# Kernel tuning notes

Measured on AMD Instinct MI355X. Metric: run time of the kernel, lower is better.

Reference implementation:

```python
import jax, jax.numpy as jnp
import numpy as np

E = 1024          # n_embed_dim
H = 64            # head_size = n_embed_dim // n_heads (16)

def setup_inputs() -> dict:
    key = jax.random.key(0)
    k_x, k_q, k_k, k_v = jax.random.split(key, 4)
    scale = 1.0 / np.sqrt(E)
    return {
        "x": jax.random.normal(k_x, (4, 2048, E), dtype=jnp.float32),
        "ln_gamma": jnp.ones((E,), jnp.float32),
        "ln_beta": jnp.zeros((E,), jnp.float32),
        # torch nn.Linear weights: [out_features, in_features]
        "Wq": jax.random.normal(k_q, (H, E), dtype=jnp.float32) * scale,
        "Wk": jax.random.normal(k_k, (H, E), dtype=jnp.float32) * scale,
        "Wv": jax.random.normal(k_v, (H, E), dtype=jnp.float32) * scale,
    }

def reference(x, ln_gamma, ln_beta, Wq, Wk, Wv):
    # LayerNorm over last dim (eps matches torch default 1e-5)
    mu = jnp.mean(x, axis=-1, keepdims=True)
    var = jnp.mean(jnp.square(x - mu), axis=-1, keepdims=True)
    xn = (x - mu) * jax.lax.rsqrt(var + 1e-5) * ln_gamma + ln_beta

    q = jnp.einsum('bse,he->bsh', xn, Wq)   # [B,S,H]
    k = jnp.einsum('bse,he->bsh', xn, Wk)
    v = jnp.einsum('bse,he->bsh', xn, Wv)

    scores = jnp.einsum('bqh,bkh->bqk', q, k) / jnp.sqrt(jnp.float32(H))
    S = x.shape[1]
    causal = jnp.tril(jnp.ones((S, S), dtype=bool))
    scores = jnp.where(causal, scores, -jnp.inf)
    attn = jax.nn.softmax(scores, axis=-1)
    return jnp.einsum('bqk,bkh->bqh', attn, v)
```

## Files before the change

kernel.cpp:

```cpp
#include <hip/hip_runtime.h>

#define E 1024
#define HH 64
#define BB 4
#define SS 2048
#define BS (BB*SS)
#define NSLOT 144

typedef unsigned short u16;
typedef short bf16x8 __attribute__((ext_vector_type(8)));
typedef float f32x4 __attribute__((ext_vector_type(4)));

#define LOG2E_O8 0.18033688011112042f

__device__ inline u16 f2bf(float f) {
    unsigned int u = __float_as_uint(f);
    unsigned int r = (u + 0x7FFFu + ((u >> 16) & 1u)) >> 16;
    return (u16)r;
}
__device__ inline float bf2f(u16 h) {
    return __uint_as_float(((unsigned int)h) << 16);
}
__device__ inline void gl2lds(const u16* g, u16* l) {
    __builtin_amdgcn_global_load_lds(
        (const __attribute__((address_space(1))) unsigned int*)g,
        (__attribute__((address_space(3))) unsigned int*)l,
        16, 0, 0);
}

__global__ __launch_bounds__(256) void ln_wcast(const float* __restrict__ x,
        const float* __restrict__ gamma, const float* __restrict__ beta,
        const float* __restrict__ Wq, const float* __restrict__ Wk,
        const float* __restrict__ Wv,
        u16* __restrict__ xn, u16* __restrict__ wc) {
    const int t = threadIdx.x;
    if (blockIdx.x < 2048) {
        const int w = t >> 6, lane = t & 63;
        const size_t row = (size_t)blockIdx.x * 4 + w;
        const int r7 = (int)(row & 7);
        const float4* xr = (const float4*)(x + row * E);
        float4 v[4];
        #pragma unroll
        for (int i = 0; i < 4; ++i) v[i] = xr[lane + 64 * i];
        float s = 0.f, sq = 0.f;
        #pragma unroll
        for (int i = 0; i < 4; ++i) {
            s  += v[i].x + v[i].y + v[i].z + v[i].w;
            sq += v[i].x*v[i].x + v[i].y*v[i].y + v[i].z*v[i].z + v[i].w*v[i].w;
        }
        #pragma unroll
        for (int off = 32; off > 0; off >>= 1) {
            s  += __shfl_xor(s,  off);
            sq += __shfl_xor(sq, off);
        }
        const float mean = s * (1.0f / E);
        const float var  = sq * (1.0f / E) - mean * mean;
        const float rstd = rsqrtf(var + 1e-5f);
        const float4* gr = (const float4*)gamma;
        const float4* br = (const float4*)beta;
        #pragma unroll
        for (int i = 0; i < 4; ++i) {
            const float4 g  = gr[lane + 64 * i];
            const float4 bt = br[lane + 64 * i];
            ushort4 o;
            o.x = f2bf((v[i].x - mean) * rstd * g.x + bt.x);
            o.y = f2bf((v[i].y - mean) * rstd * g.y + bt.y);
            o.z = f2bf((v[i].z - mean) * rstd * g.z + bt.z);
            o.w = f2bf((v[i].w - mean) * rstd * g.w + bt.w);
            const int p = lane + 64 * i;
            const int dst = (p >> 5) * 128 + ((p >> 4) & 1) * 64
                          + ((((p >> 1) & 7) ^ r7) * 8) + (p & 1) * 4;
            *(ushort4*)(xn + row * E + dst) = o;
        }
    } else {
        const int row = blockIdx.x - 2048;
        const float* src = (row < 64)  ? (Wq + (size_t)row * E)
                         : (row < 128) ? (Wk + (size_t)(row - 64) * E)
                                       : (Wv + (size_t)(row - 128) * E);
        const float sc = (row < 64) ? LOG2E_O8 : 1.0f;
        const float4 v = *(const float4*)(src + t * 4);
        ushort4 o;
        o.x = f2bf(v.x * sc); o.y = f2bf(v.y * sc);
        o.z = f2bf(v.z * sc); o.w = f2bf(v.w * sc);
        const int dst = (t >> 5) * 128 + ((t >> 4) & 1) * 64
                      + ((((t >> 1) & 7) ^ (row & 7)) * 8) + (t & 1) * 4;
        *(ushort4*)(wc + (size_t)row * E + dst) = o;
    }
}

__global__ __launch_bounds__(256) void qkv_mfma(const u16* __restrict__ xn,
        const u16* __restrict__ wc,
        u16* __restrict__ qb, u16* __restrict__ kb, u16* __restrict__ vt) {
    const int mb   = blockIdx.x >> 1;
    const int half = blockIdx.x & 1;
    const int row0 = mb * 32;
    const int t = threadIdx.x;
    const int w = t >> 6, lane = t & 63;
    const int quad = lane >> 4, r15 = lane & 15;
    const int mt = w >> 1, cgrp = w & 1;
    __shared__ u16 Xs[2][32 * 128];
    __shared__ u16 Ws[2][96 * 128];
    f32x4 acc[3] = {};
    const int xrow = mt * 16 + r15;

    const int srow = t >> 4, u = t & 15;

    auto stage = [&](int kc, int buf) {
        gl2lds(xn + (size_t)(row0 + srow) * E + kc * 128 + u * 8,
               &Xs[buf][w * 512]);
        gl2lds(xn + (size_t)(row0 + 16 + srow) * E + kc * 128 + u * 8,
               &Xs[buf][2048 + w * 512]);
        #pragma unroll
        for (int i = 0; i < 6; ++i) {
            const int wl = i * 16 + srow;
            gl2lds(wc + (size_t)(half * 96 + wl) * E + kc * 128 + u * 8,
                   &Ws[buf][i * 2048 + w * 512]);
        }
    };

    stage(0, 0);
    __syncthreads();

    for (int kc8 = 0; kc8 < 8; ++kc8) {
        const int cur = kc8 & 1;
        if (kc8 < 7) stage(kc8 + 1, cur ^ 1);
        #pragma unroll
        for (int kk = 0; kk < 4; ++kk) {
            const int hf = kk >> 1, q4 = (kk & 1) * 4 + quad;
            const bf16x8 af = *(const bf16x8*)&Xs[cur][xrow * 128 + hf * 64 + (q4 ^ (xrow & 7)) * 8];
            #pragma unroll
            for (int j = 0; j < 3; ++j) {
                const int wl = (cgrp * 3 + j) * 16 + r15;
                const bf16x8 bfr = *(const bf16x8*)&Ws[cur][wl * 128 + hf * 64 + (q4 ^ (wl & 7)) * 8];
                acc[j] = __builtin_amdgcn_mfma_f32_16x16x32_bf16(af, bfr, acc[j], 0, 0, 0);
            }
        }
        __syncthreads();
    }

    const int b    = row0 >> 11;
    const int key0 = row0 & 2047;
    #pragma unroll
    for (int j = 0; j < 3; ++j) {
        const int cg  = half * 96 + cgrp * 48 + j * 16 + r15;
        const int sel = cg >> 6;
        const int col = cg & 63;
        if (sel < 2) {
            u16* base = (sel == 0) ? qb : kb;
            #pragma unroll
            for (int r = 0; r < 4; ++r) {
                const size_t row = (size_t)row0 + mt * 16 + quad * 4 + r;
                base[row * HH + col] = f2bf(acc[j][r]);
            }
        } else {
            ushort4 pk;
            pk.x = f2bf(acc[j][0]); pk.y = f2bf(acc[j][1]);
            pk.z = f2bf(acc[j][2]); pk.w = f2bf(acc[j][3]);
            *(ushort4*)(vt + (size_t)b * HH * SS + (size_t)col * SS
                           + key0 + mt * 16 + quad * 4) = pk;
        }
    }
}

__global__ __launch_bounds__(256) void attn_partial(const u16* __restrict__ qb,
        const u16* __restrict__ kb, const u16* __restrict__ vt,
        u16* __restrict__ po, float* __restrict__ pl,
        float* __restrict__ out) {
    const int bid = blockIdx.x;
    const int b   = bid / 72;
    const int s2  = bid - b * 72;
    int a = (int)((sqrtf(4.0f * s2 + 1.0f) - 1.0f) * 0.5f);
    while ((a + 1) * (a + 2) <= s2) ++a;
    while (a * (a + 1) > s2) --a;
    const int rem = s2 - a * (a + 1);
    const int rp  = rem / (a + 1);
    const int c   = rem - rp * (a + 1);
    const int qt0 = 4 * a + 2 * rp;
    const int nc  = a + 1;
    const int t = threadIdx.x;
    const int w = t >> 6, lane = t & 63;
    const int quad = lane >> 4, r15 = lane & 15;

    __shared__ u16 Ks[4 * 64 * 64];
    __shared__ u16 VT[4 * 64 * 64];
    __shared__ u16 Ps[64 * 64];

    bf16x8 qf0[2], qf1[2];
    #pragma unroll
    for (int qi = 0; qi < 2; ++qi) {
        const size_t qrow = ((size_t)b * SS + (qt0 + qi) * 64 + w * 16 + r15) * HH;
        qf0[qi] = *(const bf16x8*)(qb + qrow + quad * 8);
        qf1[qi] = *(const bf16x8*)(qb + qrow + 32 + quad * 8);
    }

    const int ntmax = (c < a) ? 4 : (2 * rp + 2);

    {
        const int row = t >> 2, ch0 = (t & 3) * 2;
        for (int tl = 0; tl < ntmax; ++tl) {
            const int kt = (c * 4 + tl) << 6;
            const uint4* srcK = (const uint4*)(kb + ((size_t)b * SS + kt + row) * HH + ch0 * 8);
            const uint4 k0 = srcK[0], k1 = srcK[1];
            *(uint4*)&Ks[tl * 4096 + row * 64 + ((ch0    ) ^ (row & 7)) * 8] = k0;
            *(uint4*)&Ks[tl * 4096 + row * 64 + ((ch0 + 1) ^ (row & 7)) * 8] = k1;
            const uint4* srcV = (const uint4*)(vt + (size_t)b * HH * SS + (size_t)row * SS
                                               + kt + ch0 * 8);
            const uint4 v0 = srcV[0], v1 = srcV[1];
            *(uint4*)&VT[tl * 4096 + row * 64 + ((ch0    ) ^ (row & 7)) * 8] = v0;
            *(uint4*)&VT[tl * 4096 + row * 64 + ((ch0 + 1) ^ (row & 7)) * 8] = v1;
        }
    }
    __syncthreads();

    f32x4 o[2][4] = {};
    float l_[2][4] = {};

    for (int tl = 0; tl < ntmax; ++tl) {
        const int tile = c * 4 + tl;
        const u16* KsT = &Ks[tl * 4096];
        const u16* VTT = &VT[tl * 4096];

        bf16x8 kf0[4], kf1[4], vf0[4], vf1[4];
        #pragma unroll
        for (int nt = 0; nt < 4; ++nt) {
            const int krow = nt * 16 + r15;
            kf0[nt] = *(const bf16x8*)&KsT[krow * 64 + ((    quad) ^ (krow & 7)) * 8];
            kf1[nt] = *(const bf16x8*)&KsT[krow * 64 + ((4 + quad) ^ (krow & 7)) * 8];
            vf0[nt] = *(const bf16x8*)&VTT[krow * 64 + ((    quad) ^ (krow & 7)) * 8];
            vf1[nt] = *(const bf16x8*)&VTT[krow * 64 + ((4 + quad) ^ (krow & 7)) * 8];
        }

        #pragma unroll
        for (int qi = 0; qi < 2; ++qi) {
            const int qt_i = qt0 + qi;
            if (tile > qt_i) continue;

            f32x4 s4[4] = {};
            #pragma unroll
            for (int nt = 0; nt < 4; ++nt) {
                s4[nt] = __builtin_amdgcn_mfma_f32_16x16x32_bf16(qf0[qi], kf0[nt], s4[nt], 0, 0, 0);
                s4[nt] = __builtin_amdgcn_mfma_f32_16x16x32_bf16(qf1[qi], kf1[nt], s4[nt], 0, 0, 0);
            }
            if (tile == qt_i) {
                #pragma unroll
                for (int nt = 0; nt < 4; ++nt)
                    #pragma unroll
                    for (int r = 0; r < 4; ++r)
                        if (nt * 16 + r15 > w * 16 + quad * 4 + r) s4[nt][r] = -INFINITY;
            }

            float p[4][4];
            #pragma unroll
            for (int r = 0; r < 4; ++r) {
                #pragma unroll
                for (int nt = 0; nt < 4; ++nt)
                    p[nt][r] = __builtin_amdgcn_exp2f(s4[nt][r]);
                l_[qi][r] += (p[0][r] + p[1][r]) + (p[2][r] + p[3][r]);
            }

            #pragma unroll
            for (int nt = 0; nt < 4; ++nt)
                #pragma unroll
                for (int r = 0; r < 4; ++r) {
                    const int prow = w * 16 + quad * 4 + r;
                    const int col  = nt * 16 + r15;
                    Ps[prow * 64 + (((col >> 3) ^ (prow & 7)) * 8) + (col & 7)] = f2bf(p[nt][r]);
                }
            const int arow = w * 16 + r15;
            const bf16x8 pf0 = *(const bf16x8*)&Ps[arow * 64 + ((    quad) ^ (arow & 7)) * 8];
            const bf16x8 pf1 = *(const bf16x8*)&Ps[arow * 64 + ((4 + quad) ^ (arow & 7)) * 8];

            #pragma unroll
            for (int ht = 0; ht < 4; ++ht) {
                o[qi][ht] = __builtin_amdgcn_mfma_f32_16x16x32_bf16(pf0, vf0[ht], o[qi][ht], 0, 0, 0);
                o[qi][ht] = __builtin_amdgcn_mfma_f32_16x16x32_bf16(pf1, vf1[ht], o[qi][ht], 0, 0, 0);
            }
        }
    }

    #pragma unroll
    for (int qi = 0; qi < 2; ++qi)
        #pragma unroll
        for (int r = 0; r < 4; ++r) {
            l_[qi][r] += __shfl_xor(l_[qi][r], 1); l_[qi][r] += __shfl_xor(l_[qi][r], 2);
            l_[qi][r] += __shfl_xor(l_[qi][r], 4); l_[qi][r] += __shfl_xor(l_[qi][r], 8);
        }

    #pragma unroll
    for (int qi = 0; qi < 2; ++qi) {
        const int qt_i = qt0 + qi;
        if (nc == 1) {
            #pragma unroll
            for (int r = 0; r < 4; ++r) {
                const float inv = 1.0f / l_[qi][r];
                const size_t orow = ((size_t)b * SS + qt_i * 64 + w * 16 + quad * 4 + r) * HH;
                #pragma unroll
                for (int ht = 0; ht < 4; ++ht)
                    out[orow + ht * 16 + r15] = o[qi][ht][r] * inv;
            }
        } else {
            const int slot = b * NSLOT + 2 * a * (a + 1) + (2 * rp + qi) * (a + 1) + c;
            #pragma unroll
            for (int r = 0; r < 4; ++r) {
                const int q = w * 16 + quad * 4 + r;
                #pragma unroll
                for (int ht = 0; ht < 4; ++ht)
                    po[(size_t)slot * 4096 + q * 64 + ht * 16 + r15] = f2bf(o[qi][ht][r]);
                if (r15 == 0) pl[slot * 64 + q] = l_[qi][r];
            }
        }
    }
}

__global__ __launch_bounds__(256) void attn_reduce(const u16* __restrict__ po,
        const float* __restrict__ pl, float* __restrict__ out) {
    const int bid = blockIdx.x;
    const int b = bid / 112, rem = bid - b * 112;
    const int qt = 4 + (rem >> 2), qq = rem & 3;
    const int a = qt >> 2, r_ = qt & 3;
    const int nc = a + 1;
    const int sbase = b * NSLOT + 2 * a * (a + 1) + r_ * (a + 1);
    const int t = threadIdx.x;
    const int h = t & 63, qr = t >> 6;
    #pragma unroll
    for (int i = 0; i < 4; ++i) {
        const int q = qq * 16 + qr * 4 + i;
        float osum = 0.f, lsum = 0.f;
        #pragma unroll
        for (int cidx = 0; cidx < 8; ++cidx) {
            if (cidx < nc) {
                osum += bf2f(po[(size_t)(sbase + cidx) * 4096 + q * 64 + h]);
                lsum += pl[(sbase + cidx) * 64 + q];
            }
        }
        out[((size_t)b * SS + (qt << 6) + q) * HH + h] = osum / lsum;
    }
}

extern "C" void kernel_launch(void* const* d_in, const int* in_sizes, int n_in,
                              void* d_out, int out_size, void* d_ws, size_t ws_size,
                              hipStream_t stream) {
    const float* x     = (const float*)d_in[0];
    const float* gamma = (const float*)d_in[1];
    const float* beta  = (const float*)d_in[2];
    const float* Wq    = (const float*)d_in[3];
    const float* Wk    = (const float*)d_in[4];
    const float* Wv    = (const float*)d_in[5];
    float* out = (float*)d_out;

    char* p = (char*)d_ws;
    u16*   xn   = (u16*)p;                         p += (size_t)BS * E * 2;
    u16*   wc   = (u16*)p;                         p += 393216;
    u16*   qb   = (u16*)p;                         p += (size_t)BS * HH * 2;
    u16*   kb   = (u16*)p;                         p += (size_t)BS * HH * 2;
    u16*   vt   = (u16*)p;                         p += (size_t)BS * HH * 2;
    u16*   po   = (u16*)p;                         p += (size_t)BB * NSLOT * 4096 * 2;
    float* pl   = (float*)p;

    ln_wcast    <<<2048 + 192,  256, 0, stream>>>(x, gamma, beta, Wq, Wk, Wv, xn, wc);
    qkv_mfma    <<<BS / 16,     256, 0, stream>>>(xn, wc, qb, kb, vt);
    attn_partial<<<BB * 72,     256, 0, stream>>>(qb, kb, vt, po, pl, out);
    attn_reduce <<<BB * 112,    256, 0, stream>>>(po, pl, out);
}
```

Before: 119.3 us.

## Fuse split-K attention into one block per query tile with double-buffered K/V

Drops the split-KV partial kernel and its reduction kernel. Each block now owns one 64-row query tile and walks all of its causal key tiles, starting with the heaviest tiles. K/V tiles are prefetched into registers and written to a double-buffered LDS stage in pairs. This removes the partial-output round trip and one launch. The cost is only 128 blocks, and the longest block runs 32 key tiles serially, which lengthens the critical path.

```diff
diff --git a/kernel.cpp b/kernel.cpp
--- a/kernel.cpp
+++ b/kernel.cpp
@@ -5,7 +5,6 @@
 #define BB 4
 #define SS 2048
 #define BS (BB*SS)
-#define NSLOT 144
 
 typedef unsigned short u16;
 typedef short bf16x8 __attribute__((ext_vector_type(8)));
@@ -162,86 +161,91 @@
     }
 }
 
-__global__ __launch_bounds__(256) void attn_partial(const u16* __restrict__ qb,
+__global__ __launch_bounds__(256) void attn_fused(const u16* __restrict__ qb,
         const u16* __restrict__ kb, const u16* __restrict__ vt,
-        u16* __restrict__ po, float* __restrict__ pl,
         float* __restrict__ out) {
     const int bid = blockIdx.x;
-    const int b   = bid / 72;
-    const int s2  = bid - b * 72;
-    int a = (int)((sqrtf(4.0f * s2 + 1.0f) - 1.0f) * 0.5f);
-    while ((a + 1) * (a + 2) <= s2) ++a;
-    while (a * (a + 1) > s2) --a;
-    const int rem = s2 - a * (a + 1);
-    const int rp  = rem / (a + 1);
-    const int c   = rem - rp * (a + 1);
-    const int qt0 = 4 * a + 2 * rp;
-    const int nc  = a + 1;
+    const int qt  = 31 - (bid >> 2);
+    const int b   = bid & 3;
+    const int ntiles = qt + 1;
+    const int nit = (ntiles + 1) >> 1;
     const int t = threadIdx.x;
     const int w = t >> 6, lane = t & 63;
     const int quad = lane >> 4, r15 = lane & 15;
 
-    __shared__ u16 Ks[4 * 64 * 64];
-    __shared__ u16 VT[4 * 64 * 64];
+    __shared__ u16 Ks[2 * 2 * 4096];
+    __shared__ u16 VT[2 * 2 * 4096];
     __shared__ u16 Ps[64 * 64];
 
-    bf16x8 qf0[2], qf1[2];
-    #pragma unroll
-    for (int qi = 0; qi < 2; ++qi) {
-        const size_t qrow = ((size_t)b * SS + (qt0 + qi) * 64 + w * 16 + r15) * HH;
-        qf0[qi] = *(const bf16x8*)(qb + qrow + quad * 8);
-        qf1[qi] = *(const bf16x8*)(qb + qrow + 32 + quad * 8);
-    }
-
-    const int ntmax = (c < a) ? 4 : (2 * rp + 2);
-
+    bf16x8 qf0, qf1;
     {
-        const int row = t >> 2, ch0 = (t & 3) * 2;
-        for (int tl = 0; tl < ntmax; ++tl) {
-            const int kt = (c * 4 + tl) << 6;
-            const uint4* srcK = (const uint4*)(kb + ((size_t)b * SS + kt + row) * HH + ch0 * 8);
-            const uint4 k0 = srcK[0], k1 = srcK[1];
-            *(uint4*)&Ks[tl * 4096 + row * 64 + ((ch0    ) ^ (row & 7)) * 8] = k0;
-            *(uint4*)&Ks[tl * 4096 + row * 64 + ((ch0 + 1) ^ (row & 7)) * 8] = k1;
-            const uint4* srcV = (const uint4*)(vt + (size_t)b * HH * SS + (size_t)row * SS
-                                               + kt + ch0 * 8);
-            const uint4 v0 = srcV[0], v1 = srcV[1];
-            *(uint4*)&VT[tl * 4096 + row * 64 + ((ch0    ) ^ (row & 7)) * 8] = v0;
-            *(uint4*)&VT[tl * 4096 + row * 64 + ((ch0 + 1) ^ (row & 7)) * 8] = v1;
-        }
+        const size_t qrow = ((size_t)b * SS + qt * 64 + w * 16 + r15) * HH;
+        qf0 = *(const bf16x8*)(qb + qrow + quad * 8);
+        qf1 = *(const bf16x8*)(qb + qrow + 32 + quad * 8);
+    }
+
+    const int srow = t >> 2, sc0 = (t & 3) * 2;
+    struct Stg { uint4 ka, kb2, va, vb; };
+    auto ld = [&](int tile) {
+        Stg s;
+        const int kt = tile << 6;
+        const uint4* srcK = (const uint4*)(kb + ((size_t)b * SS + kt + srow) * HH + sc0 * 8);
+        s.ka = srcK[0]; s.kb2 = srcK[1];
+        const uint4* srcV = (const uint4*)(vt + (size_t)b * HH * SS + (size_t)srow * SS
+                                           + kt + sc0 * 8);
+        s.va = srcV[0]; s.vb = srcV[1];
+        return s;
+    };
+    auto wr = [&](const Stg& s, int buf, int slot) {
+        u16* kd = &Ks[(buf * 2 + slot) * 4096 + srow * 64];
+        *(uint4*)&kd[((sc0    ) ^ (srow & 7)) * 8] = s.ka;
+        *(uint4*)&kd[((sc0 + 1) ^ (srow & 7)) * 8] = s.kb2;
+        u16* vd = &VT[(buf * 2 + slot) * 4096 + srow * 64];
+        *(uint4*)&vd[((sc0    ) ^ (srow & 7)) * 8] = s.va;
+        *(uint4*)&vd[((sc0 + 1) ^ (srow & 7)) * 8] = s.vb;
+    };
+
+    {
+        Stg s0 = ld(0);
+        wr(s0, 0, 0);
+        if (1 < ntiles) { Stg s1 = ld(1); wr(s1, 0, 1); }
     }
     __syncthreads();
 
-    f32x4 o[2][4] = {};
-    float l_[2][4] = {};
-
-    for (int tl = 0; tl < ntmax; ++tl) {
-        const int tile = c * 4 + tl;
-        const u16* KsT = &Ks[tl * 4096];
-        const u16* VTT = &VT[tl * 4096];
-
-        bf16x8 kf0[4], kf1[4], vf0[4], vf1[4];
-        #pragma unroll
-        for (int nt = 0; nt < 4; ++nt) {
-            const int krow = nt * 16 + r15;
-            kf0[nt] = *(const bf16x8*)&KsT[krow * 64 + ((    quad) ^ (krow & 7)) * 8];
-            kf1[nt] = *(const bf16x8*)&KsT[krow * 64 + ((4 + quad) ^ (krow & 7)) * 8];
-            vf0[nt] = *(const bf16x8*)&VTT[krow * 64 + ((    quad) ^ (krow & 7)) * 8];
-            vf1[nt] = *(const bf16x8*)&VTT[krow * 64 + ((4 + quad) ^ (krow & 7)) * 8];
-        }
-
-        #pragma unroll
-        for (int qi = 0; qi < 2; ++qi) {
-            const int qt_i = qt0 + qi;
-            if (tile > qt_i) continue;
+    f32x4 o[4] = {};
+    float l_[4] = {};
+
+    for (int it = 0; it < nit; ++it) {
+        const int cur = it & 1;
+        const bool pf  = (it + 1 < nit);
+        const bool pf1 = (2 * it + 3 < ntiles);
+        Stg s0, s1;
+        if (pf) { s0 = ld(2 * it + 2); if (pf1) s1 = ld(2 * it + 3); }
+
+        #pragma unroll
+        for (int sl = 0; sl < 2; ++sl) {
+            const int tile = 2 * it + sl;
+            if (tile >= ntiles) break;
+            const u16* KsT = &Ks[(cur * 2 + sl) * 4096];
+            const u16* VTT = &VT[(cur * 2 + sl) * 4096];
+
+            bf16x8 kf0[4], kf1[4], vf0[4], vf1[4];
+            #pragma unroll
+            for (int nt = 0; nt < 4; ++nt) {
+                const int krow = nt * 16 + r15;
+                kf0[nt] = *(const bf16x8*)&KsT[krow * 64 + ((    quad) ^ (krow & 7)) * 8];
+                kf1[nt] = *(const bf16x8*)&KsT[krow * 64 + ((4 + quad) ^ (krow & 7)) * 8];
+                vf0[nt] = *(const bf16x8*)&VTT[krow * 64 + ((    quad) ^ (krow & 7)) * 8];
+                vf1[nt] = *(const bf16x8*)&VTT[krow * 64 + ((4 + quad) ^ (krow & 7)) * 8];
+            }
 
             f32x4 s4[4] = {};
             #pragma unroll
             for (int nt = 0; nt < 4; ++nt) {
-                s4[nt] = __builtin_amdgcn_mfma_f32_16x16x32_bf16(qf0[qi], kf0[nt], s4[nt], 0, 0, 0);
-                s4[nt] = __builtin_amdgcn_mfma_f32_16x16x32_bf16(qf1[qi], kf1[nt], s4[nt], 0, 0, 0);
-            }
-            if (tile == qt_i) {
+                s4[nt] = __builtin_amdgcn_mfma_f32_16x16x32_bf16(qf0, kf0[nt], s4[nt], 0, 0, 0);
+                s4[nt] = __builtin_amdgcn_mfma_f32_16x16x32_bf16(qf1, kf1[nt], s4[nt], 0, 0, 0);
+            }
+            if (tile == qt) {
                 #pragma unroll
                 for (int nt = 0; nt < 4; ++nt)
                     #pragma unroll
@@ -255,7 +259,7 @@
                 #pragma unroll
                 for (int nt = 0; nt < 4; ++nt)
                     p[nt][r] = __builtin_amdgcn_exp2f(s4[nt][r]);
-                l_[qi][r] += (p[0][r] + p[1][r]) + (p[2][r] + p[3][r]);
+                l_[r] += (p[0][r] + p[1][r]) + (p[2][r] + p[3][r]);
             }
 
             #pragma unroll
@@ -267,73 +271,32 @@
                     Ps[prow * 64 + (((col >> 3) ^ (prow & 7)) * 8) + (col & 7)] = f2bf(p[nt][r]);
                 }
             const int arow = w * 16 + r15;
-            const bf16x8 pf0 = *(const bf16x8*)&Ps[arow * 64 + ((    quad) ^ (arow & 7)) * 8];
-            const bf16x8 pf1 = *(const bf16x8*)&Ps[arow * 64 + ((4 + quad) ^ (arow & 7)) * 8];
+            const bf16x8 pf0_ = *(const bf16x8*)&Ps[arow * 64 + ((    quad) ^ (arow & 7)) * 8];
+            const bf16x8 pf1_ = *(const bf16x8*)&Ps[arow * 64 + ((4 + quad) ^ (arow & 7)) * 8];
 
             #pragma unroll
             for (int ht = 0; ht < 4; ++ht) {
-                o[qi][ht] = __builtin_amdgcn_mfma_f32_16x16x32_bf16(pf0, vf0[ht], o[qi][ht], 0, 0, 0);
-                o[qi][ht] = __builtin_amdgcn_mfma_f32_16x16x32_bf16(pf1, vf1[ht], o[qi][ht], 0, 0, 0);
-            }
-        }
+                o[ht] = __builtin_amdgcn_mfma_f32_16x16x32_bf16(pf0_, vf0[ht], o[ht], 0, 0, 0);
+                o[ht] = __builtin_amdgcn_mfma_f32_16x16x32_bf16(pf1_, vf1[ht], o[ht], 0, 0, 0);
+            }
+        }
+
+        if (pf) { wr(s0, cur ^ 1, 0); if (pf1) wr(s1, cur ^ 1, 1); }
+        __syncthreads();
     }
 
     #pragma unroll
-    for (int qi = 0; qi < 2; ++qi)
-        #pragma unroll
-        for (int r = 0; r < 4; ++r) {
-            l_[qi][r] += __shfl_xor(l_[qi][r], 1); l_[qi][r] += __shfl_xor(l_[qi][r], 2);
-            l_[qi][r] += __shfl_xor(l_[qi][r], 4); l_[qi][r] += __shfl_xor(l_[qi][r], 8);
-        }
-
+    for (int r = 0; r < 4; ++r) {
+        l_[r] += __shfl_xor(l_[r], 1); l_[r] += __shfl_xor(l_[r], 2);
+        l_[r] += __shfl_xor(l_[r], 4); l_[r] += __shfl_xor(l_[r], 8);
+    }
     #pragma unroll
-    for (int qi = 0; qi < 2; ++qi) {
-        const int qt_i = qt0 + qi;
-        if (nc == 1) {
-            #pragma unroll
-            for (int r = 0; r < 4; ++r) {
-                const float inv = 1.0f / l_[qi][r];
-                const size_t orow = ((size_t)b * SS + qt_i * 64 + w * 16 + quad * 4 + r) * HH;
-                #pragma unroll
-                for (int ht = 0; ht < 4; ++ht)
-                    out[orow + ht * 16 + r15] = o[qi][ht][r] * inv;
-            }
-        } else {
-            const int slot = b * NSLOT + 2 * a * (a + 1) + (2 * rp + qi) * (a + 1) + c;
-            #pragma unroll
-            for (int r = 0; r < 4; ++r) {
-                const int q = w * 16 + quad * 4 + r;
-                #pragma unroll
-                for (int ht = 0; ht < 4; ++ht)
-                    po[(size_t)slot * 4096 + q * 64 + ht * 16 + r15] = f2bf(o[qi][ht][r]);
-                if (r15 == 0) pl[slot * 64 + q] = l_[qi][r];
-            }
-        }
-    }
-}
-
-__global__ __launch_bounds__(256) void attn_reduce(const u16* __restrict__ po,
-        const float* __restrict__ pl, float* __restrict__ out) {
-    const int bid = blockIdx.x;
-    const int b = bid / 112, rem = bid - b * 112;
-    const int qt = 4 + (rem >> 2), qq = rem & 3;
-    const int a = qt >> 2, r_ = qt & 3;
-    const int nc = a + 1;
-    const int sbase = b * NSLOT + 2 * a * (a + 1) + r_ * (a + 1);
-    const int t = threadIdx.x;
-    const int h = t & 63, qr = t >> 6;
-    #pragma unroll
-    for (int i = 0; i < 4; ++i) {
-        const int q = qq * 16 + qr * 4 + i;
-        float osum = 0.f, lsum = 0.f;
-        #pragma unroll
-        for (int cidx = 0; cidx < 8; ++cidx) {
-            if (cidx < nc) {
-                osum += bf2f(po[(size_t)(sbase + cidx) * 4096 + q * 64 + h]);
-                lsum += pl[(sbase + cidx) * 64 + q];
-            }
-        }
-        out[((size_t)b * SS + (qt << 6) + q) * HH + h] = osum / lsum;
+    for (int r = 0; r < 4; ++r) {
+        const float inv = 1.0f / l_[r];
+        const size_t orow = ((size_t)b * SS + qt * 64 + w * 16 + quad * 4 + r) * HH;
+        #pragma unroll
+        for (int ht = 0; ht < 4; ++ht)
+            out[orow + ht * 16 + r15] = o[ht][r] * inv;
     }
 }
 
@@ -353,12 +316,9 @@
     u16*   wc   = (u16*)p;                         p += 393216;
     u16*   qb   = (u16*)p;                         p += (size_t)BS * HH * 2;
     u16*   kb   = (u16*)p;                         p += (size_t)BS * HH * 2;
-    u16*   vt   = (u16*)p;                         p += (size_t)BS * HH * 2;
-    u16*   po   = (u16*)p;                         p += (size_t)BB * NSLOT * 4096 * 2;
-    float* pl   = (float*)p;
-
-    ln_wcast    <<<2048 + 192,  256, 0, stream>>>(x, gamma, beta, Wq, Wk, Wv, xn, wc);
-    qkv_mfma    <<<BS / 16,     256, 0, stream>>>(xn, wc, qb, kb, vt);
-    attn_partial<<<BB * 72,     256, 0, stream>>>(qb, kb, vt, po, pl, out);
-    attn_reduce <<<BB * 112,    256, 0, stream>>>(po, pl, out);
-}
+    u16*   vt   = (u16*)p;
+
+    ln_wcast  <<<2048 + 192, 256, 0, stream>>>(x, gamma, beta, Wq, Wk, Wv, xn, wc);
+    qkv_mfma  <<<BS / 16,    256, 0, stream>>>(xn, wc, qb, kb, vt);
+    attn_fused<<<BB * 32,    256, 0, stream>>>(qb, kb, vt, out);
+}
```

Result: slower. 127.1 us (+6.5%).
